# Performance work log

Hardware: AMD Instinct MI355X
Metric: run time of the kernel (lower is better)

## Reference

```python
import jax, jax.numpy as jnp
import numpy as np

B, C, CI, H, W = 4, 256, 128, 64, 64  # batch, in_channels, inter_channels, spatial


def conv1x1(x, w, b):
    # x: [B,C,H,W], w: [O,C], b: [O] -> [B,O,H,W]
    return jnp.einsum('bchw,oc->bohw', x, w) + b[None, :, None, None]


def setup_inputs() -> dict:
    key = jax.random.key(0)
    ks = jax.random.split(key, 9)
    s = 0.02
    return {
        'x':  jax.random.normal(ks[0], (B, C, H, W), dtype=jnp.float32),
        'Wg': jax.random.normal(ks[1], (CI, C), dtype=jnp.float32) * s,
        'bg': jnp.zeros((CI,), dtype=jnp.float32),
        'Wt': jax.random.normal(ks[2], (CI, C), dtype=jnp.float32) * s,
        'bt': jnp.zeros((CI,), dtype=jnp.float32),
        'Wp': jax.random.normal(ks[3], (CI, C), dtype=jnp.float32) * s,
        'bp': jnp.zeros((CI,), dtype=jnp.float32),
        'Wo': jax.random.normal(ks[4], (C, CI), dtype=jnp.float32) * s,
        'bo': jnp.zeros((C,), dtype=jnp.float32),
    }


def reference(x, Wg, bg, Wt, bt, Wp, bp, Wo, bo):
    b, c, h, w = x.shape
    n = h * w
    g  = conv1x1(x, Wg, bg).reshape(b, -1, n)   # [B,CI,N]
    th = conv1x1(x, Wt, bt).reshape(b, -1, n)   # [B,CI,N]
    ph = conv1x1(x, Wp, bp).reshape(b, -1, n)   # [B,CI,N]
    f = jnp.einsum('bci,bcj->bij', th, ph)      # [B,N,N] unscaled scores
    a = jax.nn.softmax(f, axis=-1)
    y = jnp.einsum('bij,bcj->bci', a, g)        # [B,CI,N]
    y = y.reshape(b, -1, h, w)
    return conv1x1(y, Wo, bo) + x
```

## Files before the change

### kernel.cpp

```cpp
#include <hip/hip_runtime.h>
#include <math.h>

#define B_  4
#define C_  256
#define CI_ 128
#define N_  4096

typedef short s16x8  __attribute__((ext_vector_type(8)));
typedef float f32x4  __attribute__((ext_vector_type(4)));
typedef float f32x16 __attribute__((ext_vector_type(16)));

__device__ inline ushort f2bf(float f) {
    unsigned int u = __float_as_uint(f);
    u += 0x7FFF + ((u >> 16) & 1);
    return (ushort)(u >> 16);
}
__device__ inline float bf2f(ushort u) {
    return __uint_as_float(((unsigned int)u) << 16);
}

__device__ inline unsigned pkbf(float a, float b) {
    unsigned r;
    asm("v_cvt_pk_bf16_f32 %0, %1, %2" : "=v"(r) : "v"(a), "v"(b));
    return r;
}
__device__ inline void plswap(unsigned &x, unsigned &y) {
    asm volatile("v_permlane32_swap_b32 %0, %1" : "+v"(x), "+v"(y));
}

__device__ inline void gload_lds16(const void* g, void* l) {
    __builtin_amdgcn_global_load_lds(
        (const __attribute__((address_space(1))) unsigned int*)g,
        (__attribute__((address_space(3))) unsigned int*)l, 16, 0, 0);
}

__device__ inline void block_sync_lds() {
    asm volatile("s_waitcnt lgkmcnt(0)" ::: "memory");
    __builtin_amdgcn_s_barrier();
    asm volatile("" ::: "memory");
}

__global__ __launch_bounds__(256) void prep_kernel(
    const float* __restrict__ Wg, const float* __restrict__ Wt,
    const float* __restrict__ Wp, const float* __restrict__ Wo,
    const float* __restrict__ bg, const float* __restrict__ bt,
    const float* __restrict__ bp,
    ushort* __restrict__ Wcat, ushort* __restrict__ Wobf,
    float* __restrict__ bcat,
    const float* __restrict__ x, ushort* __restrict__ xT)
{
    __shared__ ushort Ls[64][72];
    const int bid = blockIdx.x;
    const int t = threadIdx.x;
    if (bid < 512) {
        int i = bid * 256 + t;
        if (i < 32768)       Wcat[i] = f2bf(Wg[i]);
        else if (i < 65536)  Wcat[i] = f2bf(Wt[i - 32768]);
        else if (i < 98304)  Wcat[i] = f2bf(Wp[i - 65536]);
        else if (i < 131072) Wobf[i - 98304] = f2bf(Wo[i - 98304]);
        if (i < 128)         bcat[i] = bg[i];
        else if (i < 256)    bcat[i] = bt[i - 128];
        else if (i < 384)    bcat[i] = bp[i - 256];
        return;
    }
    int idx2 = bid - 512;
    const int n0 = (idx2 & 63) * 64;
    const int c0 = ((idx2 >> 6) & 3) * 64;
    const int b  = idx2 >> 8;
    const float* xb = x + ((size_t)b * C_ + c0) * N_ + n0;
    #pragma unroll
    for (int r = 0; r < 4; r++) {
        int idx = t + 256 * r;
        int c = idx >> 4, n4 = (idx & 15) * 4;
        float4 v = *(const float4*)&xb[(size_t)c * N_ + n4];
        ushort4 o;
        o.x = f2bf(v.x); o.y = f2bf(v.y); o.z = f2bf(v.z); o.w = f2bf(v.w);
        *(ushort4*)&Ls[c][n4] = o;
    }
    __syncthreads();
    ushort* xTb = xT + ((size_t)b * N_ + n0) * C_ + c0;
    #pragma unroll
    for (int r = 0; r < 2; r++) {
        int idx = t + 256 * r;
        int n = idx >> 3, c8 = (idx & 7) * 8;
        ushort tmp[8];
        #pragma unroll
        for (int u = 0; u < 8; u++) tmp[u] = Ls[c8 + u][n];
        *(uint4*)&xTb[(size_t)n * C_ + c8] = *(uint4*)tmp;
    }
}

__global__ __launch_bounds__(256, 2) void proj_kernel(
    const ushort* __restrict__ Wcat, const float* __restrict__ bcat,
    const ushort* __restrict__ xT,
    ushort* __restrict__ g, ushort* __restrict__ tht, ushort* __restrict__ pht)
{
    __shared__ __align__(16) char smem[65536];
    const int b = blockIdx.z, mt = blockIdx.y, n0 = blockIdx.x * 128;
    const int t = threadIdx.x, wv = t >> 6, lane = t & 63;
    const int wr = wv >> 1, wc = wv & 1;
    const int g4 = lane >> 4, ln = lane & 15;

    const char* Asrc = (const char*)(Wcat + (size_t)mt * 128 * C_);
    const char* Bsrc = (const char*)(xT + ((size_t)b * N_ + n0) * C_);

    const int sr = lane >> 3;
    const int sc = (lane & 7) << 4;
    const int ssw = sc ^ (sr << 4);

    f32x4 acc[4][4];
    #pragma unroll
    for (int i = 0; i < 4; i++)
        #pragma unroll
        for (int j = 0; j < 4; j++) acc[i][j] = (f32x4){0.f, 0.f, 0.f, 0.f};

    const int rsw = (ln & 7) << 4;

#define PROJ_STAGE(bufofs, k0) do {                                          \
    _Pragma("unroll")                                                        \
    for (int r_ = 0; r_ < 4; r_++) {                                         \
        int c_   = (wv << 2) + r_;                                           \
        int row_ = (c_ << 3) + sr;                                           \
        gload_lds16(Asrc + (size_t)row_ * 512 + (k0) * 2 + ssw,              \
                    smem + (bufofs) + (c_ << 10));                           \
        gload_lds16(Bsrc + (size_t)row_ * 512 + (k0) * 2 + ssw,              \
                    smem + (bufofs) + 16384 + (c_ << 10));                   \
    }                                                                        \
} while (0)

    PROJ_STAGE(0, 0);
    int buf = 0;
    #pragma unroll
    for (int s = 0; s < 4; s++) {
        if (s < 3) {
            PROJ_STAGE(buf ^ 32768, (s + 1) * 64);
            asm volatile("s_waitcnt vmcnt(8)" ::: "memory");
        } else {
            asm volatile("s_waitcnt vmcnt(0)" ::: "memory");
        }
        __builtin_amdgcn_s_barrier();
        asm volatile("" ::: "memory");

        const char* Ab = smem + buf;
        const char* Bb = smem + buf + 16384;
        #pragma unroll
        for (int kk = 0; kk < 2; kk++) {
            s16x8 aW[4], bX[4];
            #pragma unroll
            for (int m4 = 0; m4 < 4; m4++)
                aW[m4] = *(const s16x8*)(Ab + ((wr * 64 + m4 * 16 + ln) << 7)
                                            + (((kk << 6) + (g4 << 4)) ^ rsw));
            #pragma unroll
            for (int nt = 0; nt < 4; nt++)
                bX[nt] = *(const s16x8*)(Bb + ((wc * 64 + nt * 16 + ln) << 7)
                                            + (((kk << 6) + (g4 << 4)) ^ rsw));
            __builtin_amdgcn_s_setprio(1);
            #pragma unroll
            for (int m4 = 0; m4 < 4; m4++)
                #pragma unroll
                for (int nt = 0; nt < 4; nt++)
                    acc[m4][nt] = __builtin_amdgcn_mfma_f32_16x16x32_bf16(
                        aW[m4], bX[nt], acc[m4][nt], 0, 0, 0);
            __builtin_amdgcn_s_setprio(0);
        }
        block_sync_lds();
        buf ^= 32768;
    }

    if (mt == 0) {
        ushort* ob = g + (size_t)b * CI_ * N_;
        #pragma unroll
        for (int m4 = 0; m4 < 4; m4++) {
            #pragma unroll
            for (int r = 0; r < 4; r++) {
                int m = wr * 64 + m4 * 16 + 4 * g4 + r;
                float bi = bcat[m];
                #pragma unroll
                for (int nt = 0; nt < 4; nt++) {
                    int n = n0 + wc * 64 + nt * 16 + ln;
                    ob[(size_t)m * N_ + n] = f2bf(acc[m4][nt][r] + bi);
                }
            }
        }
    } else {
        ushort* ob = (mt == 1 ? tht : pht) + (size_t)b * N_ * CI_;
        const float* bb = bcat + mt * 128;
        #pragma unroll
        for (int m4 = 0; m4 < 4; m4++) {
            int mbase = wr * 64 + m4 * 16 + 4 * g4;
            #pragma unroll
            for (int nt = 0; nt < 4; nt++) {
                int n = n0 + wc * 64 + nt * 16 + ln;
                ushort v4[4];
                #pragma unroll
                for (int r = 0; r < 4; r++)
                    v4[r] = f2bf(acc[m4][nt][r] + bb[mbase + r]);
                *(ushort4*)&ob[(size_t)n * CI_ + mbase] = *(ushort4*)v4;
            }
        }
    }
#undef PROJ_STAGE
}

__device__ inline float build_pa(const f32x16& S, s16x8& f0, s16x8& f1) {
    unsigned w[8];
    #pragma unroll
    for (int e = 0; e < 8; e++)
        w[e] = pkbf(__expf(S[2 * e]), __expf(S[2 * e + 1]));
    float ls = 0.f;
    #pragma unroll
    for (int e = 0; e < 8; e++)
        ls += __uint_as_float(w[e] << 16) + __uint_as_float(w[e] & 0xFFFF0000u);
    plswap(w[0], w[2]);
    plswap(w[1], w[3]);
    plswap(w[4], w[6]);
    plswap(w[5], w[7]);
    union { unsigned u[4]; s16x8 v; } A, B;
    A.u[0] = w[0]; A.u[1] = w[1]; A.u[2] = w[2]; A.u[3] = w[3];
    B.u[0] = w[4]; B.u[1] = w[5]; B.u[2] = w[6]; B.u[3] = w[7];
    f0 = A.v; f1 = B.v;
    return ls;
}

#define STAGE_KV(bufofs, jsrc) do {                                          \
    _Pragma("unroll")                                                        \
    for (int r_ = 0; r_ < 4; r_++) {                                         \
        int c_   = (wv << 2) + r_;                                           \
        int row_ = (c_ << 2) + kr;                                           \
        int src_ = (((jsrc) + row_) << 8) + (kc ^ ((row_ & 7) << 4));        \
        gload_lds16(kB + src_, smemB + (bufofs) + (c_ << 10));               \
    }                                                                        \
    _Pragma("unroll")                                                        \
    for (int r_ = 0; r_ < 4; r_++) {                                         \
        int c_   = (wv << 2) + r_;                                           \
        int row_ = (c_ << 3) + vr;                                           \
        int src_ = row_ * (N_ * 2) + ((jsrc) << 1) + (vc ^ ((row_ & 7) << 4));\
        gload_lds16(vB + src_, smemB + (bufofs) + 16384 + (c_ << 10));       \
    }                                                                        \
} while (0)

#define NC_ 4
#define JC_ (N_ / NC_)

__global__ __launch_bounds__(256, 2) void attn_mfma_kernel(
    const ushort* __restrict__ qn,
    const ushort* __restrict__ kn,
    const ushort* __restrict__ vm,
    ushort* __restrict__ Opart,
    float* __restrict__ lbuf)
{
    __shared__ __align__(16) char smemB[65536];

    constexpr int NI = N_ / 128;
    constexpr int nb = NI * NC_ * B_;
    int flat = (blockIdx.z * NC_ + blockIdx.y) * NI + blockIdx.x;
    int nf   = (flat & 7) * (nb / 8) + (flat >> 3);
    const int i0    = (nf % NI) * 128;
    const int chunk = (nf / NI) % NC_;
    const int b     = nf / (NI * NC_);
    const int jbase = chunk * JC_;

    const int t    = threadIdx.x;
    const int wv   = t >> 6;
    const int lane = t & 63;
    const int n32  = lane & 31;
    const int h    = lane >> 5;
    const int swz  = (n32 & 7) << 4;

    const char* kB = (const char*)(kn + (size_t)b * N_ * CI_);
    const char* vB = (const char*)(vm + (size_t)b * CI_ * N_);

    const ushort* qb = qn + ((size_t)b * N_ + i0) * CI_;
    s16x8 aQ[8];
    #pragma unroll
    for (int kk = 0; kk < 8; kk++)
        aQ[kk] = *(const s16x8*)(qb + (size_t)(32 * wv + n32) * CI_ + 16 * kk + 8 * h);

    f32x16 Oacc[4];
    #pragma unroll
    for (int dt = 0; dt < 4; dt++)
        #pragma unroll
        for (int e = 0; e < 16; e++) Oacc[dt][e] = 0.f;
    float lsum = 0.f;

    const int kr = lane >> 4;
    const int kc = (lane & 15) << 4;
    const int vr = lane >> 3;
    const int vc = (lane & 7) << 4;

    STAGE_KV(0, jbase);
    int buf = 0;
    for (int jt = jbase; jt < jbase + JC_; jt += 64) {
        if (jt + 64 < jbase + JC_) {
            STAGE_KV(buf ^ 32768, jt + 64);
            asm volatile("s_waitcnt vmcnt(8)" ::: "memory");
        } else {
            asm volatile("s_waitcnt vmcnt(0)" ::: "memory");
        }
        __builtin_amdgcn_s_barrier();
        asm volatile("" ::: "memory");

        const char* Kc = smemB + buf;
        const char* Vc = smemB + buf + 16384;

        s16x8 pa[4];
        {
            f32x16 S0;
            #pragma unroll
            for (int e = 0; e < 16; e++) S0[e] = 0.f;
            __builtin_amdgcn_s_setprio(1);
            #pragma unroll
            for (int kk = 0; kk < 8; kk++) {
                s16x8 aK = *(const s16x8*)(Kc + (n32 << 8) + (((kk << 5) + (h << 4)) ^ swz));
                S0 = __builtin_amdgcn_mfma_f32_32x32x16_bf16(aK, aQ[kk], S0, 0, 0, 0);
            }
            __builtin_amdgcn_s_setprio(0);
            lsum += build_pa(S0, pa[0], pa[1]);
        }
        {
            f32x16 S1;
            #pragma unroll
            for (int e = 0; e < 16; e++) S1[e] = 0.f;
            __builtin_amdgcn_s_setprio(1);
            #pragma unroll
            for (int kk = 0; kk < 8; kk++) {
                s16x8 aK = *(const s16x8*)(Kc + 8192 + (n32 << 8) + (((kk << 5) + (h << 4)) ^ swz));
                S1 = __builtin_amdgcn_mfma_f32_32x32x16_bf16(aK, aQ[kk], S1, 0, 0, 0);
            }
            __builtin_amdgcn_s_setprio(0);
            lsum += build_pa(S1, pa[2], pa[3]);
        }

        __builtin_amdgcn_s_setprio(1);
        #pragma unroll
        for (int dt = 0; dt < 4; dt++) {
            #pragma unroll
            for (int kk = 0; kk < 4; kk++) {
                s16x8 bV = *(const s16x8*)(Vc + ((32 * dt + n32) << 7)
                                              + (((kk << 5) + (h << 4)) ^ swz));
                Oacc[dt] = __builtin_amdgcn_mfma_f32_32x32x16_bf16(pa[kk], bV, Oacc[dt], 0, 0, 0);
            }
        }
        __builtin_amdgcn_s_setprio(0);

        block_sync_lds();
        buf ^= 32768;
    }

    ushort* Ob = Opart + (size_t)chunk * (B_ * N_ * CI_) + ((size_t)b * N_ + i0) * CI_;
    #pragma unroll
    for (int rg = 0; rg < 16; rg++) {
        int R = (rg & 3) + 8 * (rg >> 2) + 4 * h;
        int q = 32 * wv + R;
        #pragma unroll
        for (int dt = 0; dt < 4; dt++)
            Ob[(size_t)q * CI_ + 32 * dt + n32] = f2bf(Oacc[dt][rg]);
    }
    float ot  = __shfl_xor(lsum, 32);
    float tot = lsum + ot;
    if (h == 0)
        lbuf[((size_t)chunk * B_ + b) * N_ + i0 + 32 * wv + n32] = tot;
}

__global__ __launch_bounds__(256, 2) void outgemm_kernel(
    const ushort* __restrict__ Wobf, const float* __restrict__ bo,
    const ushort* __restrict__ Opart, const float* __restrict__ lbuf,
    const float* __restrict__ x, float* __restrict__ out)
{
    __shared__ __align__(16) char smem[65536];
    __shared__ float invL[128];
    const int b = blockIdx.z, m0 = blockIdx.y * 128, n0 = blockIdx.x * 128;
    const int t = threadIdx.x, wv = t >> 6, lane = t & 63;
    const int wr = wv >> 1, wc = wv & 1;
    const int g4 = lane >> 4, ln = lane & 15;
    const size_t cs = (size_t)B_ * N_ * CI_;

    {
        const char* Wsrc = (const char*)(Wobf + (size_t)m0 * CI_);
        int srl = lane >> 4;
        int scl = (lane & 15) << 4;
        #pragma unroll
        for (int r = 0; r < 8; r++) {
            int c   = (wv << 3) + r;
            int row = (c << 2) + srl;
            gload_lds16(Wsrc + (size_t)row * 256 + (scl ^ ((row & 15) << 4)),
                        smem + (c << 10));
        }
    }

    if (t < 128) {
        float ls = 0.f;
        #pragma unroll
        for (int c = 0; c < NC_; c++)
            ls += lbuf[((size_t)c * B_ + b) * N_ + n0 + t];
        invL[t] = 1.0f / ls;
    }
    block_sync_lds();

    {
        #pragma unroll
        for (int r = 0; r < 8; r++) {
            int c   = t + 256 * r;
            int row = c >> 4;
            int col = (c & 15) << 4;
            size_t obase = ((size_t)b * N_ + n0 + row) * CI_ + (c & 15) * 8;
            float inv = invL[row];
            float osum[8];
            #pragma unroll
            for (int u = 0; u < 8; u++) osum[u] = 0.f;
            #pragma unroll
            for (int cc = 0; cc < NC_; cc++) {
                ushort oc[8];
                *(uint4*)oc = *(const uint4*)&Opart[(size_t)cc * cs + obase];
                #pragma unroll
                for (int u = 0; u < 8; u++) osum[u] += bf2f(oc[u]);
            }
            ushort yo[8];
            #pragma unroll
            for (int u = 0; u < 8; u++) yo[u] = f2bf(osum[u] * inv);
            *(uint4*)(smem + 32768 + row * 256 + (col ^ ((row & 15) << 4))) = *(uint4*)yo;
        }
    }
    asm volatile("s_waitcnt vmcnt(0)" ::: "memory");
    block_sync_lds();

    f32x4 acc[4][4];
    #pragma unroll
    for (int i = 0; i < 4; i++)
        #pragma unroll
        for (int j = 0; j < 4; j++) acc[i][j] = (f32x4){0.f, 0.f, 0.f, 0.f};

    const int rsw = ln << 4;
    #pragma unroll
    for (int kk = 0; kk < 4; kk++) {
        s16x8 aW[4], bY[4];
        #pragma unroll
        for (int m4 = 0; m4 < 4; m4++)
            aW[m4] = *(const s16x8*)(smem + ((wr * 64 + m4 * 16 + ln) << 8)
                                          + (((kk << 6) + (g4 << 4)) ^ rsw));
        #pragma unroll
        for (int nt = 0; nt < 4; nt++)
            bY[nt] = *(const s16x8*)(smem + 32768 + ((wc * 64 + nt * 16 + ln) << 8)
                                          + (((kk << 6) + (g4 << 4)) ^ rsw));
        __builtin_amdgcn_s_setprio(1);
        #pragma unroll
        for (int m4 = 0; m4 < 4; m4++)
            #pragma unroll
            for (int nt = 0; nt < 4; nt++)
                acc[m4][nt] = __builtin_amdgcn_mfma_f32_16x16x32_bf16(
                    aW[m4], bY[nt], acc[m4][nt], 0, 0, 0);
        __builtin_amdgcn_s_setprio(0);
    }

    float* outb = out + (size_t)b * C_ * N_;
    const float* xb = x + (size_t)b * C_ * N_;
    #pragma unroll
    for (int m4 = 0; m4 < 4; m4++) {
        #pragma unroll
        for (int r = 0; r < 4; r++) {
            int m = m0 + wr * 64 + m4 * 16 + 4 * g4 + r;
            float bi = bo[m];
            #pragma unroll
            for (int nt = 0; nt < 4; nt++) {
                size_t idx = (size_t)m * N_ + n0 + wc * 64 + nt * 16 + ln;
                outb[idx] = acc[m4][nt][r] + bi + xb[idx];
            }
        }
    }
}

extern "C" void kernel_launch(void* const* d_in, const int* in_sizes, int n_in,
                              void* d_out, int out_size, void* d_ws, size_t ws_size,
                              hipStream_t stream) {
    const float* x  = (const float*)d_in[0];
    const float* Wg = (const float*)d_in[1];
    const float* bg = (const float*)d_in[2];
    const float* Wt = (const float*)d_in[3];
    const float* bt = (const float*)d_in[4];
    const float* Wp = (const float*)d_in[5];
    const float* bp = (const float*)d_in[6];
    const float* Wo = (const float*)d_in[7];
    const float* bo = (const float*)d_in[8];
    float* out = (float*)d_out;

    char* w = (char*)d_ws;
    ushort* xT    = (ushort*)w;
    ushort* Opart = (ushort*)w;
    ushort* g     = (ushort*)(w + 16777216);
    ushort* tht   = (ushort*)(w + 20971520);
    ushort* pht   = (ushort*)(w + 25165824);
    ushort* Wcat  = (ushort*)(w + 29360128);
    ushort* Wobf  = (ushort*)(w + 29556736);
    float*  bcat  = (float*) (w + 29622272);
    float*  lbuf  = (float*) (w + 29623808);

    dim3 blk(256);
    prep_kernel<<<1536, blk, 0, stream>>>(Wg, Wt, Wp, Wo, bg, bt, bp,
                                          Wcat, Wobf, bcat, x, xT);
    proj_kernel<<<dim3(N_ / 128, 3, B_), blk, 0, stream>>>(Wcat, bcat, xT, g, tht, pht);
    attn_mfma_kernel<<<dim3(N_ / 128, NC_, B_), blk, 0, stream>>>(tht, pht, g, Opart, lbuf);
    outgemm_kernel<<<dim3(N_ / 128, C_ / 128, B_), blk, 0, stream>>>(Wobf, bo, Opart, lbuf, x, out);
}
```

Baseline: 145.4 us.

## Fold log2e into theta projection, use exp2, and widen LDS swizzle for K/V

The theta projection output is pre-multiplied by log2(e), so the attention kernel can use the raw v_exp_f32 (exp2) instead of __expf, which drops one multiply per score. The row sum is now taken from fp32 exponentials through a tree reduction instead of unpacking bf16 values. K and V tiles in LDS get a 16-way XOR swizzle over 256-byte rows (V packs two channel rows per LDS row) to cut bank conflicts on the MFMA operand reads. The risks are a slightly different rounding of the softmax denominator and added address arithmetic.

```diff
diff --git a/kernel.cpp b/kernel.cpp
--- a/kernel.cpp
+++ b/kernel.cpp
@@ -27,6 +27,11 @@
 __device__ inline void plswap(unsigned &x, unsigned &y) {
     asm volatile("v_permlane32_swap_b32 %0, %1" : "+v"(x), "+v"(y));
 }
+__device__ inline float fexp2(float x) {
+    float r;
+    asm("v_exp_f32 %0, %1" : "=v"(r) : "v"(x));
+    return r;
+}
 
 __device__ inline void gload_lds16(const void* g, void* l) {
     __builtin_amdgcn_global_load_lds(
@@ -39,6 +44,8 @@
     __builtin_amdgcn_s_barrier();
     asm volatile("" ::: "memory");
 }
+
+#define LOG2E 1.44269504f
 
 __global__ __launch_bounds__(256) void prep_kernel(
     const float* __restrict__ Wg, const float* __restrict__ Wt,
@@ -185,6 +192,7 @@
     } else {
         ushort* ob = (mt == 1 ? tht : pht) + (size_t)b * N_ * CI_;
         const float* bb = bcat + mt * 128;
+        const float scale = (mt == 1) ? LOG2E : 1.0f;
         #pragma unroll
         for (int m4 = 0; m4 < 4; m4++) {
             int mbase = wr * 64 + m4 * 16 + 4 * g4;
@@ -194,7 +202,7 @@
                 ushort v4[4];
                 #pragma unroll
                 for (int r = 0; r < 4; r++)
-                    v4[r] = f2bf(acc[m4][nt][r] + bb[mbase + r]);
+                    v4[r] = f2bf((acc[m4][nt][r] + bb[mbase + r]) * scale);
                 *(ushort4*)&ob[(size_t)n * CI_ + mbase] = *(ushort4*)v4;
             }
         }
@@ -202,15 +210,20 @@
 #undef PROJ_STAGE
 }
 
+
 __device__ inline float build_pa(const f32x16& S, s16x8& f0, s16x8& f1) {
+    float e[16];
+    #pragma unroll
+    for (int i = 0; i < 16; i++) e[i] = fexp2(S[i]);
+    float t0[8];
+    #pragma unroll
+    for (int i = 0; i < 8; i++) t0[i] = e[2 * i] + e[2 * i + 1];
+    float t1a = (t0[0] + t0[1]) + (t0[2] + t0[3]);
+    float t1b = (t0[4] + t0[5]) + (t0[6] + t0[7]);
+    float ls = t1a + t1b;
     unsigned w[8];
     #pragma unroll
-    for (int e = 0; e < 8; e++)
-        w[e] = pkbf(__expf(S[2 * e]), __expf(S[2 * e + 1]));
-    float ls = 0.f;
-    #pragma unroll
-    for (int e = 0; e < 8; e++)
-        ls += __uint_as_float(w[e] << 16) + __uint_as_float(w[e] & 0xFFFF0000u);
+    for (int i = 0; i < 8; i++) w[i] = pkbf(e[2 * i], e[2 * i + 1]);
     plswap(w[0], w[2]);
     plswap(w[1], w[3]);
     plswap(w[4], w[6]);
@@ -226,16 +239,19 @@
     _Pragma("unroll")                                                        \
     for (int r_ = 0; r_ < 4; r_++) {                                         \
         int c_   = (wv << 2) + r_;                                           \
-        int row_ = (c_ << 2) + kr;                                           \
-        int src_ = (((jsrc) + row_) << 8) + (kc ^ ((row_ & 7) << 4));        \
-        gload_lds16(kB + src_, smemB + (bufofs) + (c_ << 10));               \
+        int row_ = (c_ << 2) + srw;                                          \
+        int so_  = slt ^ (row_ & 15);                                        \
+        gload_lds16(kB + (((jsrc) + row_) << 8) + (so_ << 4),                \
+                    smemB + (bufofs) + (c_ << 10));                          \
     }                                                                        \
     _Pragma("unroll")                                                        \
     for (int r_ = 0; r_ < 4; r_++) {                                         \
         int c_   = (wv << 2) + r_;                                           \
-        int row_ = (c_ << 3) + vr;                                           \
-        int src_ = row_ * (N_ * 2) + ((jsrc) << 1) + (vc ^ ((row_ & 7) << 4));\
-        gload_lds16(vB + src_, smemB + (bufofs) + 16384 + (c_ << 10));       \
+        int rr_  = (c_ << 2) + srw;                                          \
+        int so_  = slt ^ (rr_ & 15);                                         \
+        int d_   = (rr_ << 1) + (so_ >> 3);                                  \
+        gload_lds16(vB + (size_t)d_ * (N_ * 2) + ((jsrc) << 1) + ((so_ & 7) << 4), \
+                    smemB + (bufofs) + 16384 + (c_ << 10));                  \
     }                                                                        \
 } while (0)
 
@@ -265,7 +281,9 @@
     const int lane = t & 63;
     const int n32  = lane & 31;
     const int h    = lane >> 5;
-    const int swz  = (n32 & 7) << 4;
+
+    const int kswz = (n32 & 15) << 4;
+    const int vswz = ((n32 >> 1) & 15) << 4;
 
     const char* kB = (const char*)(kn + (size_t)b * N_ * CI_);
     const char* vB = (const char*)(vm + (size_t)b * CI_ * N_);
@@ -283,10 +301,8 @@
         for (int e = 0; e < 16; e++) Oacc[dt][e] = 0.f;
     float lsum = 0.f;
 
-    const int kr = lane >> 4;
-    const int kc = (lane & 15) << 4;
-    const int vr = lane >> 3;
-    const int vc = (lane & 7) << 4;
+    const int srw = lane >> 4;
+    const int slt = lane & 15;
 
     STAGE_KV(0, jbase);
     int buf = 0;
@@ -311,7 +327,8 @@
             __builtin_amdgcn_s_setprio(1);
             #pragma unroll
             for (int kk = 0; kk < 8; kk++) {
-                s16x8 aK = *(const s16x8*)(Kc + (n32 << 8) + (((kk << 5) + (h << 4)) ^ swz));
+                s16x8 aK = *(const s16x8*)(Kc + (n32 << 8)
+                                              + (((kk << 5) + (h << 4)) ^ kswz));
                 S0 = __builtin_amdgcn_mfma_f32_32x32x16_bf16(aK, aQ[kk], S0, 0, 0, 0);
             }
             __builtin_amdgcn_s_setprio(0);
@@ -324,7 +341,8 @@
             __builtin_amdgcn_s_setprio(1);
             #pragma unroll
             for (int kk = 0; kk < 8; kk++) {
-                s16x8 aK = *(const s16x8*)(Kc + 8192 + (n32 << 8) + (((kk << 5) + (h << 4)) ^ swz));
+                s16x8 aK = *(const s16x8*)(Kc + ((32 + n32) << 8)
+                                              + (((kk << 5) + (h << 4)) ^ kswz));
                 S1 = __builtin_amdgcn_mfma_f32_32x32x16_bf16(aK, aQ[kk], S1, 0, 0, 0);
             }
             __builtin_amdgcn_s_setprio(0);
@@ -334,10 +352,11 @@
         __builtin_amdgcn_s_setprio(1);
         #pragma unroll
         for (int dt = 0; dt < 4; dt++) {
+            int vrow = (dt << 4) + (n32 >> 1);
             #pragma unroll
             for (int kk = 0; kk < 4; kk++) {
-                s16x8 bV = *(const s16x8*)(Vc + ((32 * dt + n32) << 7)
-                                              + (((kk << 5) + (h << 4)) ^ swz));
+                s16x8 bV = *(const s16x8*)(Vc + (vrow << 8)
+                    + ((((n32 & 1) << 7) + (kk << 5) + (h << 4)) ^ vswz));
                 Oacc[dt] = __builtin_amdgcn_mfma_f32_32x32x16_bf16(pa[kk], bV, Oacc[dt], 0, 0, 0);
             }
         }
```

New measurement: 141.4 us (median of 2 runs). 2.7% less time.
